# Performance work log

Measured on AMD Instinct MI355X. Metric: run time of the kernel, lower is better.

Reference implementation:

```python
import jax, jax.numpy as jnp
import numpy as np

SCALE = 0.08838834764831845  # 1/sqrt(128)
NEG_INF = -1e30


def setup_inputs() -> dict:
    key = jax.random.key(0)
    ks = jax.random.split(key, 6)
    S, Hq, Hkv, D, NB, BS, BMAX, X = 32, 32, 8, 128, 4096, 16, 128, 8
    query = jax.random.normal(ks[0], (S, Hq, D), jnp.float32)
    key_cache = jax.random.normal(ks[1], (NB, Hkv, D // X, BS, X), jnp.float32)
    value_cache = jax.random.normal(ks[2], (NB, Hkv, D, BS), jnp.float32)
    block_tables = jax.random.randint(ks[3], (S, BMAX), 0, NB, dtype=jnp.int32)
    seq_lens = jax.random.randint(ks[4], (S,), 1, BMAX * BS + 1, dtype=jnp.int32)
    alibi_slopes = jax.random.uniform(ks[5], (Hq,), jnp.float32)
    query_start_len = jnp.arange(S + 1, dtype=jnp.int32)  # every seq is a 1-token decode
    return dict(query_ptr=query, key_cache_ptr=key_cache, value_cache_ptr=value_cache,
                block_tables_ptr=block_tables, seq_lens_ptr=seq_lens,
                alibi_slopes_ptr=alibi_slopes, query_start_len_ptr=query_start_len)


def reference(query_ptr, key_cache_ptr, value_cache_ptr, block_tables_ptr,
              seq_lens_ptr, alibi_slopes_ptr, query_start_len_ptr):
    S, Bmax = block_tables_ptr.shape
    NB, Hkv, D0, BS, X = key_cache_ptr.shape
    D = D0 * X
    Hq = query_ptr.shape[1]
    G = Hq // Hkv  # queries per kv head
    Kmax = Bmax * BS

    # de-interleave vLLM K layout [NB,Hkv,D//x,BS,x] -> [NB,Hkv,BS,D]; K[d] = cache[.., d//x, tok, d%x]
    K = key_cache_ptr.transpose(0, 1, 3, 2, 4).reshape(NB, Hkv, BS, D).astype(jnp.float32)
    V = value_cache_ptr.transpose(0, 1, 3, 2).astype(jnp.float32)  # [NB,Hkv,BS,D]

    qstart = query_start_len_ptr[:-1]
    qlen = query_start_len_ptr[1:] - qstart

    q = query_ptr[qstart].astype(jnp.float32).reshape(S, Hkv, G, D)  # one decode token per seq

    # block-table-driven KV gather: [S,Bmax,Hkv,BS,D] -> [S,Hkv,Kmax,D]
    Kg = K[block_tables_ptr].transpose(0, 2, 1, 3, 4).reshape(S, Hkv, Kmax, D)
    Vg = V[block_tables_ptr].transpose(0, 2, 1, 3, 4).reshape(S, Hkv, Kmax, D)

    scores = SCALE * jnp.einsum('shgd,shkd->shgk', q, Kg)  # [S,Hkv,G,Kmax]

    pos = jnp.arange(Kmax, dtype=jnp.float32)
    ctx = (seq_lens_ptr.astype(jnp.float32) - 1.0)[:, None, None, None]
    slopes = alibi_slopes_ptr.reshape(Hkv, G)  # head idx = kv_head*G + q
    bias = slopes[None, :, :, None] * (pos[None, None, None, :] - ctx)
    valid = (jnp.arange(Kmax)[None, :] < seq_lens_ptr[:, None])[:, None, None, :]
    scores = jnp.where(valid, scores + bias, NEG_INF)

    m = jnp.max(scores, axis=-1, keepdims=True)
    p = jnp.exp(scores - m) * valid  # online-softmax numerator
    l = jnp.sum(p, axis=-1, keepdims=True)
    acc = jnp.einsum('shgk,shkd->shgd', p, Vg)
    out = acc / (l + 1e-10)  # matches acc/(L + 1e-10) in source

    decode = (qlen == 1).astype(query_ptr.dtype)  # seqs with query_len>1 are skipped (zeros)
    out = out.reshape(S, Hq, D).astype(query_ptr.dtype) * decode[:, None, None]
    return jnp.zeros_like(query_ptr).at[qstart].set(out)
```

## Files before the change

### kernel.cpp

```cpp
#include <hip/hip_runtime.h>

#define SCALE_F 0.08838834764831845f
#define NEG_INF -1e30f

constexpr int S    = 32;
constexpr int Hq   = 32;
constexpr int Hkv  = 8;
constexpr int G    = 4;
constexpr int D    = 128;
constexpr int BS   = 16;
constexpr int BMAX = 128;
constexpr int KMAX = BMAX * BS;

template<int PARTS>
__global__ __launch_bounds__(256, 3)
void attn_wave_kernel(const float* __restrict__ q_ptr,
                      const float* __restrict__ kc,
                      const float* __restrict__ vc,
                      const int*   __restrict__ bt,
                      const int*   __restrict__ slens,
                      const float* __restrict__ slopes,
                      float* __restrict__ part_acc,
                      float* __restrict__ part_m,
                      float* __restrict__ part_l)
{
    constexpr int CHUNKW = KMAX / PARTS;
    constexpr int CPW    = CHUNKW / BS;

    __shared__ float sm_p[4][G * CHUNKW];

    const int wid  = threadIdx.x >> 6;
    const int lane = threadIdx.x & 63;
    const int gw   = blockIdx.x * 4 + wid;
    const int part = gw % PARTS;
    const int sh   = gw / PARTS;
    const int h    = sh & (Hkv - 1);
    const int s    = sh >> 3;

    const int seq_len   = slens[s];
    const int num_parts = (seq_len + CHUNKW - 1) / CHUNKW;
    if (part >= num_parts) return;

    float* smp = sm_p[wid];

    int phys[CPW];
    #pragma unroll
    for (int i = 0; i < CPW; ++i) phys[i] = bt[s * BMAX + part * CPW + i];

    const float ctx  = (float)(seq_len - 1);
    const int   pos0 = part * CHUNKW;

    const int o4 = lane >> 4;
    const int t  = lane & 15;

    const float wslope = slopes[h * G + (t & 3)];

    float4 qa[G], qb[G];
    #pragma unroll
    for (int g = 0; g < G; ++g) {
        const float* qp = q_ptr + ((size_t)(s * Hq + h * G + g) * D + t * 8);
        qa[g] = ((const float4*)qp)[0];
        qb[g] = ((const float4*)qp)[1];
    }

    float4 kA[2][4], kB[2][4];
    {
        const float* kbase = kc + ((((size_t)phys[0] * Hkv + h) * (D / 8) + t) * BS) * 8;
        #pragma unroll
        for (int j2 = 0; j2 < 4; ++j2) {
            const float* kp = kbase + (j2 * 4 + o4) * 8;
            kA[0][j2] = ((const float4*)kp)[0];
            kB[0][j2] = ((const float4*)kp)[1];
        }
    }

    #pragma unroll
    for (int i = 0; i < CPW; ++i) {
        const int cb = i & 1;
        if (i + 1 < CPW) {
            const float* kbase = kc + ((((size_t)phys[i + 1] * Hkv + h) * (D / 8) + t) * BS) * 8;
            #pragma unroll
            for (int j2 = 0; j2 < 4; ++j2) {
                const float* kp = kbase + (j2 * 4 + o4) * 8;
                kA[cb ^ 1][j2] = ((const float4*)kp)[0];
                kB[cb ^ 1][j2] = ((const float4*)kp)[1];
            }
        }
        #pragma unroll
        for (int j2 = 0; j2 < 4; ++j2) {
            float sc0 = qa[0].x*kA[cb][j2].x + qa[0].y*kA[cb][j2].y + qa[0].z*kA[cb][j2].z + qa[0].w*kA[cb][j2].w
                      + qb[0].x*kB[cb][j2].x + qb[0].y*kB[cb][j2].y + qb[0].z*kB[cb][j2].z + qb[0].w*kB[cb][j2].w;
            float sc1 = qa[1].x*kA[cb][j2].x + qa[1].y*kA[cb][j2].y + qa[1].z*kA[cb][j2].z + qa[1].w*kA[cb][j2].w
                      + qb[1].x*kB[cb][j2].x + qb[1].y*kB[cb][j2].y + qb[1].z*kB[cb][j2].z + qb[1].w*kB[cb][j2].w;
            float sc2 = qa[2].x*kA[cb][j2].x + qa[2].y*kA[cb][j2].y + qa[2].z*kA[cb][j2].z + qa[2].w*kA[cb][j2].w
                      + qb[2].x*kB[cb][j2].x + qb[2].y*kB[cb][j2].y + qb[2].z*kB[cb][j2].z + qb[2].w*kB[cb][j2].w;
            float sc3 = qa[3].x*kA[cb][j2].x + qa[3].y*kA[cb][j2].y + qa[3].z*kA[cb][j2].z + qa[3].w*kA[cb][j2].w
                      + qb[3].x*kB[cb][j2].x + qb[3].y*kB[cb][j2].y + qb[3].z*kB[cb][j2].z + qb[3].w*kB[cb][j2].w;
            #pragma unroll
            for (int msk = 8; msk >= 1; msk >>= 1) {
                sc0 += __shfl_xor(sc0, msk, 16);
                sc1 += __shfl_xor(sc1, msk, 16);
                sc2 += __shfl_xor(sc2, msk, 16);
                sc3 += __shfl_xor(sc3, msk, 16);
            }
            if (t < 4) {
                const int pl   = i * BS + j2 * 4 + o4;
                const int kpos = pos0 + pl;
                const float scv = (t == 0) ? sc0 : (t == 1) ? sc1 : (t == 2) ? sc2 : sc3;
                smp[t * CHUNKW + pl] =
                    (kpos < seq_len) ? (SCALE_F * scv + wslope * ((float)kpos - ctx)) : NEG_INF;
            }
        }
    }

    const int d0 = lane;
    float4 vreg[2][2][4];
    {
        const float* vb = vc + ((size_t)phys[0] * Hkv + h) * D * BS;
        #pragma unroll
        for (int c = 0; c < 4; ++c) {
            vreg[0][0][c] = ((const float4*)(vb + (size_t)d0 * BS))[c];
            vreg[0][1][c] = ((const float4*)(vb + (size_t)(d0 + 64) * BS))[c];
        }
    }

    {
        const int gS = lane >> 4;
        const int u  = lane & 15;
        float* rowp = smp + gS * CHUNKW;

        float4 sv = ((const float4*)(rowp + u * 4))[0];
        float m = fmaxf(fmaxf(sv.x, sv.y), fmaxf(sv.z, sv.w));
        #pragma unroll
        for (int msk = 8; msk >= 1; msk >>= 1) m = fmaxf(m, __shfl_xor(m, msk, 16));

        float4 pv;
        pv.x = __expf(sv.x - m);
        pv.y = __expf(sv.y - m);
        pv.z = __expf(sv.z - m);
        pv.w = __expf(sv.w - m);
        float l = pv.x + pv.y + pv.z + pv.w;
        ((float4*)(rowp + u * 4))[0] = pv;
        #pragma unroll
        for (int msk = 8; msk >= 1; msk >>= 1) l += __shfl_xor(l, msk, 16);

        if (u == 0) {
            part_m[(sh * PARTS + part) * G + gS] = m;
            part_l[(sh * PARTS + part) * G + gS] = l;
        }
    }

    float acc0[G] = {0.f, 0.f, 0.f, 0.f};
    float acc1[G] = {0.f, 0.f, 0.f, 0.f};

    #pragma unroll
    for (int i = 0; i < CPW; ++i) {
        const int cb = i & 1;
        if (i + 1 < CPW) {
            const float* vb = vc + ((size_t)phys[i + 1] * Hkv + h) * D * BS;
            #pragma unroll
            for (int c = 0; c < 4; ++c) {
                vreg[cb ^ 1][0][c] = ((const float4*)(vb + (size_t)d0 * BS))[c];
                vreg[cb ^ 1][1][c] = ((const float4*)(vb + (size_t)(d0 + 64) * BS))[c];
            }
        }
        #pragma unroll
        for (int g = 0; g < G; ++g) {
            const float4* pp = (const float4*)(smp + g * CHUNKW + i * BS);
            #pragma unroll
            for (int c = 0; c < 4; ++c) {
                const float4 p4 = pp[c];
                acc0[g] += p4.x * vreg[cb][0][c].x + p4.y * vreg[cb][0][c].y
                         + p4.z * vreg[cb][0][c].z + p4.w * vreg[cb][0][c].w;
                acc1[g] += p4.x * vreg[cb][1][c].x + p4.y * vreg[cb][1][c].y
                         + p4.z * vreg[cb][1][c].z + p4.w * vreg[cb][1][c].w;
            }
        }
    }

    float* outp = part_acc + (size_t)(sh * PARTS + part) * G * D;
    #pragma unroll
    for (int g = 0; g < G; ++g) {
        outp[g * D + d0]      = acc0[g];
        outp[g * D + d0 + 64] = acc1[g];
    }
}

__global__ __launch_bounds__(512)
void attn_reduce_kernel(const float* __restrict__ part_acc,
                        const float* __restrict__ part_m,
                        const float* __restrict__ part_l,
                        const int*   __restrict__ slens,
                        float* __restrict__ out,
                        int parts, int chunk)
{
    const int sh  = blockIdx.x;
    const int s   = sh / Hkv;
    const int tid = threadIdx.x;
    const int g   = tid >> 7;
    const int d   = tid & 127;

    const int seq_len = slens[s];
    const int np = min(parts, (seq_len + chunk - 1) / chunk);

    float M = NEG_INF;
    for (int p = 0; p < np; ++p)
        M = fmaxf(M, part_m[(sh * parts + p) * G + g]);
    float L = 0.f, acc = 0.f;
    for (int p = 0; p < np; ++p) {
        const float w = __expf(part_m[(sh * parts + p) * G + g] - M);
        L += w * part_l[(sh * parts + p) * G + g];
        acc += w * part_acc[((size_t)(sh * parts + p) * G + g) * D + d];
    }
    out[(size_t)(sh * G + g) * D + d] = acc / (L + 1e-10f);
}

extern "C" void kernel_launch(void* const* d_in, const int* in_sizes, int n_in,
                              void* d_out, int out_size, void* d_ws, size_t ws_size,
                              hipStream_t stream)
{
    const float* q   = (const float*)d_in[0];
    const float* kc  = (const float*)d_in[1];
    const float* vc  = (const float*)d_in[2];
    const int*   bt  = (const int*)d_in[3];
    const int*   sl  = (const int*)d_in[4];
    const float* slp = (const float*)d_in[5];

    auto ws_need = [](int p) {
        return (size_t)S * Hkv * p * G * (D + 2) * sizeof(float);
    };
    int parts = 32;
    while (parts > 4 && ws_need(parts) > ws_size) parts >>= 1;
    const int chunk = KMAX / parts;

    float* part_acc = (float*)d_ws;
    float* part_m   = part_acc + (size_t)S * Hkv * parts * G * D;
    float* part_l   = part_m   + (size_t)S * Hkv * parts * G;

    const dim3 grid1(S * Hkv * parts / 4);
    switch (parts) {
    case 32: attn_wave_kernel<32><<<grid1, 256, 0, stream>>>(q, kc, vc, bt, sl, slp, part_acc, part_m, part_l); break;
    case 16: attn_wave_kernel<16><<<grid1, 256, 0, stream>>>(q, kc, vc, bt, sl, slp, part_acc, part_m, part_l); break;
    case 8:  attn_wave_kernel<8> <<<grid1, 256, 0, stream>>>(q, kc, vc, bt, sl, slp, part_acc, part_m, part_l); break;
    default: attn_wave_kernel<4> <<<grid1, 256, 0, stream>>>(q, kc, vc, bt, sl, slp, part_acc, part_m, part_l); break;
    }
    attn_reduce_kernel<<<S * Hkv, 512, 0, stream>>>(
        part_acc, part_m, part_l, sl, (float*)d_out, parts, chunk);
}
```

Baseline: 483.5 us.

## Reduce split-K partitions to 8 with multi-chunk softmax and padded shared rows

Cuts the number of KV partitions per (sequence, kv-head) from 32 to 8, so each wave processes a 256-token chunk. The softmax stage loops over several 64-wide sub-chunks per lane, and the shared score rows get 4 floats of padding to reduce LDS bank conflicts. The aim is to lower partial-result traffic and reduce-kernel work, and to reduce early-exit waves on short sequences. In exchange there are far fewer waves in the grid, longer serial work per wave, and a lower occupancy hint in launch_bounds.

```diff
diff --git a/kernel.cpp b/kernel.cpp
--- a/kernel.cpp
+++ b/kernel.cpp
@@ -13,7 +13,7 @@
 constexpr int KMAX = BMAX * BS;
 
 template<int PARTS>
-__global__ __launch_bounds__(256, 3)
+__global__ __launch_bounds__(256, 2)
 void attn_wave_kernel(const float* __restrict__ q_ptr,
                       const float* __restrict__ kc,
                       const float* __restrict__ vc,
@@ -25,9 +25,11 @@
                       float* __restrict__ part_l)
 {
     constexpr int CHUNKW = KMAX / PARTS;
+    constexpr int NCH    = CHUNKW / 64;
     constexpr int CPW    = CHUNKW / BS;
-
-    __shared__ float sm_p[4][G * CHUNKW];
+    constexpr int CPAD   = CHUNKW + 4;
+
+    __shared__ float sm_p[4][G * CPAD];
 
     const int wid  = threadIdx.x >> 6;
     const int lane = threadIdx.x & 63;
@@ -107,7 +109,7 @@
                 const int pl   = i * BS + j2 * 4 + o4;
                 const int kpos = pos0 + pl;
                 const float scv = (t == 0) ? sc0 : (t == 1) ? sc1 : (t == 2) ? sc2 : sc3;
-                smp[t * CHUNKW + pl] =
+                smp[t * CPAD + pl] =
                     (kpos < seq_len) ? (SCALE_F * scv + wslope * ((float)kpos - ctx)) : NEG_INF;
             }
         }
@@ -127,20 +129,29 @@
     {
         const int gS = lane >> 4;
         const int u  = lane & 15;
-        float* rowp = smp + gS * CHUNKW;
-
-        float4 sv = ((const float4*)(rowp + u * 4))[0];
-        float m = fmaxf(fmaxf(sv.x, sv.y), fmaxf(sv.z, sv.w));
+        float* rowp = smp + gS * CPAD;
+
+        float4 sv[NCH];
+        float m = NEG_INF;
+        #pragma unroll
+        for (int w = 0; w < NCH; ++w) {
+            sv[w] = ((const float4*)(rowp + u * 4 + w * 64))[0];
+            m = fmaxf(m, fmaxf(fmaxf(sv[w].x, sv[w].y), fmaxf(sv[w].z, sv[w].w)));
+        }
         #pragma unroll
         for (int msk = 8; msk >= 1; msk >>= 1) m = fmaxf(m, __shfl_xor(m, msk, 16));
 
-        float4 pv;
-        pv.x = __expf(sv.x - m);
-        pv.y = __expf(sv.y - m);
-        pv.z = __expf(sv.z - m);
-        pv.w = __expf(sv.w - m);
-        float l = pv.x + pv.y + pv.z + pv.w;
-        ((float4*)(rowp + u * 4))[0] = pv;
+        float l = 0.f;
+        #pragma unroll
+        for (int w = 0; w < NCH; ++w) {
+            float4 pv;
+            pv.x = __expf(sv[w].x - m);
+            pv.y = __expf(sv[w].y - m);
+            pv.z = __expf(sv[w].z - m);
+            pv.w = __expf(sv[w].w - m);
+            l += pv.x + pv.y + pv.z + pv.w;
+            ((float4*)(rowp + u * 4 + w * 64))[0] = pv;
+        }
         #pragma unroll
         for (int msk = 8; msk >= 1; msk >>= 1) l += __shfl_xor(l, msk, 16);
 
@@ -166,7 +177,7 @@
         }
         #pragma unroll
         for (int g = 0; g < G; ++g) {
-            const float4* pp = (const float4*)(smp + g * CHUNKW + i * BS);
+            const float4* pp = (const float4*)(smp + g * CPAD + i * BS);
             #pragma unroll
             for (int c = 0; c < 4; ++c) {
                 const float4 p4 = pp[c];
@@ -229,7 +240,7 @@
     auto ws_need = [](int p) {
         return (size_t)S * Hkv * p * G * (D + 2) * sizeof(float);
     };
-    int parts = 32;
+    int parts = 8;
     while (parts > 4 && ws_need(parts) > ws_size) parts >>= 1;
     const int chunk = KMAX / parts;
 
@@ -239,8 +250,6 @@
 
     const dim3 grid1(S * Hkv * parts / 4);
     switch (parts) {
-    case 32: attn_wave_kernel<32><<<grid1, 256, 0, stream>>>(q, kc, vc, bt, sl, slp, part_acc, part_m, part_l); break;
-    case 16: attn_wave_kernel<16><<<grid1, 256, 0, stream>>>(q, kc, vc, bt, sl, slp, part_acc, part_m, part_l); break;
     case 8:  attn_wave_kernel<8> <<<grid1, 256, 0, stream>>>(q, kc, vc, bt, sl, slp, part_acc, part_m, part_l); break;
     default: attn_wave_kernel<4> <<<grid1, 256, 0, stream>>>(q, kc, vc, bt, sl, slp, part_acc, part_m, part_l); break;
     }
```

After: 471.1 us. 2.6% less time.
